# Kernel optimization log

Hardware: AMD Instinct MI355X
Metric: run time of the kernel (lower is better)

The kernel has to match this reference:

```python
import jax, jax.numpy as jnp
import numpy as np

BH, W, C, NHEAD = 512, 256, 128, 4
HEAD_DIM = C // NHEAD
EPS = 1e-5


def _xavier(key, shape):
    fan_out, fan_in = shape
    lim = np.sqrt(6.0 / (fan_in + fan_out)).astype(np.float32)
    return jax.random.uniform(key, shape, jnp.float32, -lim, lim)


def setup_inputs() -> dict:
    key = jax.random.key(0)
    ks = jax.random.split(key, 4)
    return {
        "feat_left": jax.random.normal(ks[0], (BH, W, C), jnp.float32),
        "feat_right": jax.random.normal(ks[1], (BH, W, C), jnp.float32),
        "l_proj_weight": _xavier(ks[2], (2 * C, C)),
        "r_proj_weight": _xavier(ks[3], (2 * C, C)),
        "l_proj_bias": jnp.zeros((2 * C,), jnp.float32),
        "r_proj_bias": jnp.zeros((2 * C,), jnp.float32),
        "l_out_weight": _xavier(jax.random.fold_in(key, 10), (C, C)),
        "l_out_bias": jnp.zeros((C,), jnp.float32),
        "r_out_weight": _xavier(jax.random.fold_in(key, 11), (C, C)),
        "r_out_bias": jnp.zeros((C,), jnp.float32),
        "norm_weight": jnp.ones((C,), jnp.float32),
        "norm_bias": jnp.zeros((C,), jnp.float32),
    }


def _layernorm(x, w, b):
    mu = jnp.mean(x, axis=-1, keepdims=True)
    var = jnp.mean(jnp.square(x - mu), axis=-1, keepdims=True)
    return (x - mu) * jax.lax.rsqrt(var + EPS) * w + b


def reference(feat_left, feat_right, l_proj_weight, r_proj_weight,
              l_proj_bias, r_proj_bias, l_out_weight, l_out_bias,
              r_out_weight, r_out_bias, norm_weight, norm_bias):
    bh, w, c = feat_left.shape
    e, hd = NHEAD, HEAD_DIM

    l_n = _layernorm(feat_left, norm_weight, norm_bias)
    r_n = _layernorm(feat_right, norm_weight, norm_bias)

    l_kv = l_n @ l_proj_weight.T + l_proj_bias
    r_kv = r_n @ r_proj_weight.T + r_proj_bias
    l_k, l_v = jnp.split(l_kv, 2, axis=-1)
    r_k, r_v = jnp.split(r_kv, 2, axis=-1)

    l_k = l_k.reshape(bh, w, e, hd)
    r_k = r_k.reshape(bh, w, e, hd)
    l_v = l_v.reshape(bh, w, e, hd)
    r_v = r_v.reshape(bh, w, e, hd)

    # shared score matrix [bh, heads, w_left, w_right]
    attn = jnp.einsum('nwec,nvec->newv', l_k, r_k) * 0.1

    # left attends over right positions (softmax over last axis)
    sm_l = jax.nn.softmax(attn, axis=-1)
    out_l = jnp.einsum('newv,nvec->nwec', sm_l, r_v).reshape(bh, w, c)

    # right attends over left positions (softmax over w axis of same scores)
    sm_r = jax.nn.softmax(attn, axis=2)
    out_r = jnp.einsum('newv,nwec->nvec', sm_r, l_v).reshape(bh, w, c)

    out_l = out_l @ l_out_weight.T + l_out_bias
    out_r = out_r @ r_out_weight.T + r_out_bias

    return feat_left + out_l, feat_right + out_r
```

## Files before the change

kernel.cpp:

```cpp
#include <hip/hip_runtime.h>
#include <hip/hip_bf16.h>

#define BH   512
#define NW   256
#define CC   128
#define TOK  (BH * NW)

typedef __attribute__((ext_vector_type(8))) short short8;
typedef __attribute__((ext_vector_type(4))) float f32x4;
typedef __attribute__((ext_vector_type(4))) int   i32x4;
typedef __attribute__((ext_vector_type(4))) unsigned short us4;
typedef __attribute__((ext_vector_type(2))) unsigned int u32x2;
typedef unsigned short ushort_t;

static __device__ __forceinline__ f32x4 mfma16(short8 a, short8 b, f32x4 c) {
    return __builtin_amdgcn_mfma_f32_16x16x32_bf16(a, b, c, 0, 0, 0);
}

static __device__ __forceinline__ unsigned int pk2(float a, float b) {
    __hip_bfloat162 h = __float22bfloat162_rn(make_float2(a, b));
    return *reinterpret_cast<unsigned int*>(&h);
}
static __device__ __forceinline__ ushort_t f2bf(float f) {
    unsigned int u = __float_as_uint(f);
    u = (u + 0x7fffu + ((u >> 16) & 1u)) >> 16;
    return (ushort_t)u;
}
#if __has_builtin(__builtin_amdgcn_exp2f)
static __device__ __forceinline__ float exp2_fast(float x) { return __builtin_amdgcn_exp2f(x); }
#else
static __device__ __forceinline__ float exp2_fast(float x) { return exp2f(x); }
#endif

__global__ __launch_bounds__(256)
void k_prep(const float* __restrict__ WpL, const float* __restrict__ WpR,
            const float* __restrict__ bpL, const float* __restrict__ bpR,
            const float* __restrict__ WoL, const float* __restrict__ WoR,
            const float* __restrict__ nw,  const float* __restrict__ nb,
            ushort_t* __restrict__ Wb, float* __restrict__ bias2,
            ushort_t* __restrict__ WoB)
{
    if (blockIdx.x < 8) {
        const int gid = blockIdx.x * 256 + threadIdx.x;
        const int row = gid >> 2;
        const int q   = gid & 3;
        const int side = row >> 8;
        const int o    = row & 255;
        const float* Wp = side ? WpR : WpL;
        const float* bp = side ? bpR : bpL;
        const float* wr = Wp + (size_t)o * 128 + q * 32;

        float acc = 0.f;
#pragma unroll
        for (int g = 0; g < 4; ++g) {
            const int c = q * 32 + g * 8;
            float4 wa = *(const float4*)(wr + g * 8);
            float4 wb = *(const float4*)(wr + g * 8 + 4);
            float4 ga = *(const float4*)(nw + c);
            float4 gb = *(const float4*)(nw + c + 4);
            float4 ba = *(const float4*)(nb + c);
            float4 bb = *(const float4*)(nb + c + 4);
            acc += wa.x*ba.x + wa.y*ba.y + wa.z*ba.z + wa.w*ba.w
                 + wb.x*bb.x + wb.y*bb.y + wb.z*bb.z + wb.w*bb.w;
            u32x2 o0, o1;
            o0[0] = pk2(wa.x*ga.x, wa.y*ga.y);
            o0[1] = pk2(wa.z*ga.z, wa.w*ga.w);
            o1[0] = pk2(wb.x*gb.x, wb.y*gb.y);
            o1[1] = pk2(wb.z*gb.z, wb.w*gb.w);
            *(u32x2*)(Wb + (size_t)row * 128 + c)     = o0;
            *(u32x2*)(Wb + (size_t)row * 128 + c + 4) = o1;
        }
        acc += __shfl_xor(acc, 1);
        acc += __shfl_xor(acc, 2);
        if (q == 0) bias2[row] = bp[o] + acc;
    } else {
        const int idx  = (blockIdx.x - 8) * 256 + threadIdx.x;
        const int row2 = idx >> 2;
        const int q    = idx & 3;
        const int side = row2 >> 7;
        const int o    = row2 & 127;
        const float* Wo = side ? WoR : WoL;
        const float* wr = Wo + (size_t)o * 128 + q * 32;
#pragma unroll
        for (int g = 0; g < 4; ++g) {
            float4 wa = *(const float4*)(wr + g * 8);
            float4 wb = *(const float4*)(wr + g * 8 + 4);
            u32x2 o0, o1;
            o0[0] = pk2(wa.x, wa.y); o0[1] = pk2(wa.z, wa.w);
            o1[0] = pk2(wb.x, wb.y); o1[1] = pk2(wb.z, wb.w);
            *(u32x2*)(WoB + (size_t)row2 * 128 + q * 32 + g * 8)     = o0;
            *(u32x2*)(WoB + (size_t)row2 * 128 + q * 32 + g * 8 + 4) = o1;
        }
    }
}

__global__ __launch_bounds__(512)
void k_ln_proj(const float* __restrict__ featL, const float* __restrict__ featR,
               const ushort_t* __restrict__ Wb, const float* __restrict__ bias2,
               ushort_t* __restrict__ kvL,      ushort_t* __restrict__ kvR)
{
    const int side = blockIdx.y;
    const float* feat = side ? featR : featL;
    const ushort_t* W = Wb + side * 32768;
    const float* b2   = bias2 + side * 256;
    ushort_t*    kv   = side ? kvR : kvL;

    const int m0  = blockIdx.x * 64;
    const int tid = threadIdx.x;
    const int wid = tid >> 6, lane = tid & 63, l16 = lane & 15, lh = lane >> 4;
    const int wn  = wid * 32;

    __shared__ ushort_t Asm[64][136];
    __shared__ ushort_t kvS[64][260];

    const int row = tid >> 3, q = tid & 7;
    const float* fr = feat + (size_t)(m0 + row) * CC + q * 16;
    float x[16];
#pragma unroll
    for (int i = 0; i < 4; ++i) {
        float4 v = *(const float4*)(fr + i * 4);
        x[i*4+0]=v.x; x[i*4+1]=v.y; x[i*4+2]=v.z; x[i*4+3]=v.w;
    }

    short8 Bf[8];
#pragma unroll
    for (int kk = 0; kk < 4; ++kk)
#pragma unroll
        for (int tn = 0; tn < 2; ++tn)
            Bf[kk*2 + tn] = *(const short8*)(W + (size_t)(wn + tn*16 + l16) * CC + kk*32 + lh*8);
    float4 bias[2];
#pragma unroll
    for (int tn = 0; tn < 2; ++tn)
        bias[tn] = *(const float4*)(b2 + wn + tn*16 + lh*4);

    {
        float s = 0.f, s2 = 0.f;
#pragma unroll
        for (int i = 0; i < 16; ++i) { s += x[i]; s2 += x[i]*x[i]; }
#pragma unroll
        for (int m = 1; m < 8; m <<= 1) { s += __shfl_xor(s, m); s2 += __shfl_xor(s2, m); }
        float mu   = s * (1.f / 128.f);
        float var  = s2 * (1.f / 128.f) - mu * mu;
        float rstd = rsqrtf(var + 1e-5f);
        float a = rstd, bsh = -mu * rstd;
#pragma unroll
        for (int g = 0; g < 2; ++g) {
            i32x4 o;
#pragma unroll
            for (int k = 0; k < 4; ++k)
                o[k] = (int)pk2(x[g*8 + 2*k] * a + bsh, x[g*8 + 2*k + 1] * a + bsh);
            *(i32x4*)&Asm[row][q * 16 + g * 8] = o;
        }
    }
    __syncthreads();

    f32x4 acc[4][2];
#pragma unroll
    for (int mt = 0; mt < 4; ++mt)
#pragma unroll
        for (int tn = 0; tn < 2; ++tn)
            acc[mt][tn] = (f32x4){0.f, 0.f, 0.f, 0.f};

#pragma unroll
    for (int kk = 0; kk < 4; ++kk) {
        short8 a[4];
#pragma unroll
        for (int mt = 0; mt < 4; ++mt)
            a[mt] = *(const short8*)&Asm[mt*16 + l16][kk*32 + lh*8];
#pragma unroll
        for (int tn = 0; tn < 2; ++tn)
#pragma unroll
            for (int mt = 0; mt < 4; ++mt)
                acc[mt][tn] = mfma16(Bf[kk*2 + tn], a[mt], acc[mt][tn]);
    }

    const float kscale = (side == 0 && wn < 128) ? 0.14426950408889634f : 1.0f;
#pragma unroll
    for (int mt = 0; mt < 4; ++mt)
#pragma unroll
        for (int tn = 0; tn < 2; ++tn) {
            const int r    = mt*16 + l16;
            const int slot = (wn >> 2) + tn*4 + lh;
            float v0 = (acc[mt][tn][0] + bias[tn].x) * kscale;
            float v1 = (acc[mt][tn][1] + bias[tn].y) * kscale;
            float v2 = (acc[mt][tn][2] + bias[tn].z) * kscale;
            float v3 = (acc[mt][tn][3] + bias[tn].w) * kscale;
            u32x2 wv;
            wv[0] = pk2(v0, v1);
            wv[1] = pk2(v2, v3);
            *(u32x2*)&kvS[r][slot * 4] = wv;
        }
    __syncthreads();

#pragma unroll
    for (int it = 0; it < 8; ++it) {
        int u = it * 512 + tid;
        int r = u >> 6, sl = u & 63;
        u32x2 wv = *(const u32x2*)&kvS[r][sl * 4];
        *(u32x2*)(kv + (size_t)(m0 + r) * 256 + sl * 4) = wv;
    }
}

template<int BF16OUT>
__global__ __launch_bounds__(512, 4)
void k_attn(const ushort_t* __restrict__ kvL, const ushort_t* __restrict__ kvR,
            float* __restrict__ outFBase, ushort_t* __restrict__ outBBase)
{
    const int bx   = blockIdx.x;
    const int work = (bx & 7) * 512 + (bx >> 3);
    const int n    = work >> 3;
    const int e    = (work >> 1) & 3;
    const int dir  = work & 1;
    const ushort_t* kvA = dir ? kvR : kvL;
    const ushort_t* kvB = dir ? kvL : kvR;

    const int tid = threadIdx.x;
    const int wid = tid >> 6, lane = tid & 63, l16 = lane & 15, lh = lane >> 4;
    const int W0 = wid * 32;
    const int kcls = (l16 >> 1) & 3;

    __shared__ ushort_t kB[256][32];
    __shared__ ushort_t vT[32][280];
    __shared__ ushort_t pL[8][32][32];

    {
        const ushort_t* src = kvB + (size_t)n * 256 * 256 + e * 32;
#pragma unroll
        for (int p = 0; p < 2; ++p) {
            int u = tid + p * 512;
            int r = u >> 2, slot = u & 3;
            *(i32x4*)&kB[r][(slot ^ ((r >> 1) & 3)) << 3] =
                *(const i32x4*)(src + (size_t)r * 256 + slot * 8);
        }
    }
    {
        const ushort_t* src = kvB + (size_t)n * 256 * 256 + 128 + e * 32;
#pragma unroll
        for (int u4 = 0; u4 < 4; ++u4) {
            int unit = tid + u4 * 512;
            int cp = unit & 15, vp = unit >> 4;
            unsigned int w0 = *(const unsigned int*)(src + (size_t)(vp*2    ) * 256 + cp*2);
            unsigned int w1 = *(const unsigned int*)(src + (size_t)(vp*2 + 1) * 256 + cp*2);
            *(unsigned int*)&vT[cp*2    ][vp*2] = (w0 & 0xffffu) | (w1 << 16);
            *(unsigned int*)&vT[cp*2 + 1][vp*2] = (w0 >> 16) | (w1 & 0xffff0000u);
        }
    }
    short8 aK[2];
#pragma unroll
    for (int tr = 0; tr < 2; ++tr)
        aK[tr] = *(const short8*)(kvA + (size_t)(n*256 + W0 + tr*16 + l16) * 256 + e*32 + lh*8);

    short8 ones;
#pragma unroll
    for (int i = 0; i < 8; ++i) ones[i] = (short)0x3F80;

    __syncthreads();

    f32x4 oacc[2][2];
#pragma unroll
    for (int tr = 0; tr < 2; ++tr)
#pragma unroll
        for (int ct = 0; ct < 2; ++ct)
            oacc[tr][ct] = (f32x4){0.f, 0.f, 0.f, 0.f};
    f32x4 lacc[2] = {(f32x4){0.f,0.f,0.f,0.f}, (f32x4){0.f,0.f,0.f,0.f}};

#pragma unroll 2
    for (int nc = 0; nc < 8; ++nc) {
        const int vc0 = nc * 32;

        short8 bk0 = *(const short8*)&kB[vc0      + l16][(lh ^ kcls) << 3];
        short8 bk1 = *(const short8*)&kB[vc0 + 16 + l16][(lh ^ kcls) << 3];
        f32x4 s[2][2];
#pragma unroll
        for (int tr = 0; tr < 2; ++tr) {
            s[tr][0] = mfma16(bk0, aK[tr], (f32x4){0.f,0.f,0.f,0.f});
            s[tr][1] = mfma16(bk1, aK[tr], (f32x4){0.f,0.f,0.f,0.f});
        }

#pragma unroll
        for (int tr = 0; tr < 2; ++tr) {
            const int prow = tr*16 + l16;
#pragma unroll
            for (int tc = 0; tc < 2; ++tc) {
                float p0 = exp2_fast(s[tr][tc][0]);
                float p1 = exp2_fast(s[tr][tc][1]);
                float p2 = exp2_fast(s[tr][tc][2]);
                float p3 = exp2_fast(s[tr][tc][3]);
                u32x2 w;
                w[0] = pk2(p0, p1);
                w[1] = pk2(p2, p3);
                const int sL   = 2*tc + (lh >> 1);
                const int pcol = ((sL ^ kcls) << 3) + ((lh & 1) << 2);
                *(u32x2*)&pL[wid][prow][pcol] = w;
            }
        }

        short8 aP[2], bV[2];
#pragma unroll
        for (int tr = 0; tr < 2; ++tr)
            aP[tr] = *(const short8*)&pL[wid][tr*16 + l16][(lh ^ kcls) << 3];
#pragma unroll
        for (int ct = 0; ct < 2; ++ct)
            bV[ct] = *(const short8*)&vT[ct*16 + l16][vc0 + lh*8];
#pragma unroll
        for (int tr = 0; tr < 2; ++tr) {
#pragma unroll
            for (int ct = 0; ct < 2; ++ct)
                oacc[tr][ct] = mfma16(bV[ct], aP[tr], oacc[tr][ct]);
            lacc[tr] = mfma16(ones, aP[tr], lacc[tr]);
        }
    }

#pragma unroll
    for (int tr = 0; tr < 2; ++tr) {
        float rinv = 1.f / lacc[tr][0];
        const int token = n * 256 + W0 + tr*16 + l16;
        if (BF16OUT) {
            ushort_t* outB = outBBase + (size_t)dir * TOK * CC;
#pragma unroll
            for (int ct = 0; ct < 2; ++ct) {
                us4 o;
#pragma unroll
                for (int j = 0; j < 4; ++j)
                    o[j] = f2bf(oacc[tr][ct][j] * rinv);
                *(us4*)(outB + (size_t)token * CC + e*32 + ct*16 + lh*4) = o;
            }
        } else {
            float* outF = outFBase + (size_t)dir * TOK * CC;
#pragma unroll
            for (int ct = 0; ct < 2; ++ct) {
                float4 o;
                o.x = oacc[tr][ct][0] * rinv;
                o.y = oacc[tr][ct][1] * rinv;
                o.z = oacc[tr][ct][2] * rinv;
                o.w = oacc[tr][ct][3] * rinv;
                *(float4*)(outF + (size_t)token * CC + e*32 + ct*16 + lh*4) = o;
            }
        }
    }
}

__global__ __launch_bounds__(512)
void k_outproj_fast(float* __restrict__ outBase, const ushort_t* __restrict__ aoutBase,
                    const float* __restrict__ featL, const float* __restrict__ featR,
                    const ushort_t* __restrict__ WoB,
                    const float* __restrict__ boL, const float* __restrict__ boR)
{
    const int side = blockIdx.y;
    float* io = outBase + (size_t)side * TOK * CC;
    const float* feat = side ? featR : featL;
    const ushort_t* Wo = WoB + side * 16384;
    const float* bo   = side ? boR : boL;

    const int m0 = blockIdx.x * 64;
    const int tid = threadIdx.x;
    const int wid = tid >> 6, lane = tid & 63, l16 = lane & 15, lh = lane >> 4;
    const int wm = (wid >> 2) * 32;
    const int wn = (wid & 3) * 32;

    __shared__ ushort_t Asm[64][136];

    short8 Bf[8];
#pragma unroll
    for (int kk = 0; kk < 4; ++kk)
#pragma unroll
        for (int tn = 0; tn < 2; ++tn)
            Bf[kk*2 + tn] = *(const short8*)(Wo + (size_t)(wn + tn*16 + l16) * CC + kk*32 + lh*8);
    float4 bias4[2];
#pragma unroll
    for (int nt = 0; nt < 2; ++nt)
        bias4[nt] = *(const float4*)(bo + wn + nt*16 + lh*4);

    {
        const ushort_t* src = aoutBase + (size_t)side * TOK * CC;
#pragma unroll
        for (int i = 0; i < 2; ++i) {
            int u = tid + i * 512;
            int r = u >> 4, c0 = (u & 15) * 8;
            *(i32x4*)&Asm[r][c0] = *(const i32x4*)(src + (size_t)(m0 + r) * CC + c0);
        }
    }
    __syncthreads();

    f32x4 acc[2][2];
#pragma unroll
    for (int tr = 0; tr < 2; ++tr)
#pragma unroll
        for (int nt = 0; nt < 2; ++nt)
            acc[tr][nt] = (f32x4){0.f, 0.f, 0.f, 0.f};

#pragma unroll
    for (int kk = 0; kk < 4; ++kk) {
        short8 a[2];
#pragma unroll
        for (int tr = 0; tr < 2; ++tr)
            a[tr] = *(const short8*)&Asm[wm + tr*16 + l16][kk*32 + lh*8];
#pragma unroll
        for (int tr = 0; tr < 2; ++tr)
#pragma unroll
            for (int nt = 0; nt < 2; ++nt)
                acc[tr][nt] = mfma16(Bf[kk*2 + nt], a[tr], acc[tr][nt]);
    }

#pragma unroll
    for (int tr = 0; tr < 2; ++tr) {
        const int token = m0 + wm + tr*16 + l16;
#pragma unroll
        for (int nt = 0; nt < 2; ++nt) {
            const int f0 = wn + nt*16 + lh*4;
            float4 ff = *(const float4*)(feat + (size_t)token * CC + f0);
            float4 o;
            o.x = acc[tr][nt][0] + bias4[nt].x + ff.x;
            o.y = acc[tr][nt][1] + bias4[nt].y + ff.y;
            o.z = acc[tr][nt][2] + bias4[nt].z + ff.z;
            o.w = acc[tr][nt][3] + bias4[nt].w + ff.w;
            *(float4*)(io + (size_t)token * CC + f0) = o;
        }
    }
}

__global__ __launch_bounds__(512, 4)
void k_outproj_slow(float* __restrict__ outBase,
                    const float* __restrict__ featL, const float* __restrict__ featR,
                    const float* __restrict__ WoL,   const float* __restrict__ WoR,
                    const float* __restrict__ boL,   const float* __restrict__ boR)
{
    const int side = blockIdx.y;
    float* io = outBase + (size_t)side * TOK * CC;
    const float* feat = side ? featR : featL;
    const float* Wo   = side ? WoR   : WoL;
    const float* bo   = side ? boR   : boL;

    const int m0 = blockIdx.x * 64;
    const int tid = threadIdx.x;
    const int wid = tid >> 6, lane = tid & 63, l16 = lane & 15, lh = lane >> 4;
    const int wm = (wid >> 2) * 32;
    const int wn = (wid & 3) * 32;

    __shared__ ushort_t Asm[64][136];
    __shared__ ushort_t Wsm[128][136];

    float4 bias4[2];
#pragma unroll
    for (int nt = 0; nt < 2; ++nt)
        bias4[nt] = *(const float4*)(bo + wn + nt*16 + lh*4);

#pragma unroll
    for (int i = 0; i < 8; ++i) {
        int u = tid + i * 512;
        int r = u >> 5, c4 = (u & 31) * 4;
        float4 w4 = *(const float4*)(Wo + (size_t)r * CC + c4);
        u32x2 wv; wv[0] = pk2(w4.x, w4.y); wv[1] = pk2(w4.z, w4.w);
        *(u32x2*)&Wsm[r][c4] = wv;
    }
#pragma unroll
    for (int i = 0; i < 4; ++i) {
        int u = tid + i * 512;
        int r = u >> 5, c4 = (u & 31) * 4;
        float4 a4 = *(const float4*)(io + (size_t)(m0 + r) * CC + c4);
        u32x2 av; av[0] = pk2(a4.x, a4.y); av[1] = pk2(a4.z, a4.w);
        *(u32x2*)&Asm[r][c4] = av;
    }
    __syncthreads();

    f32x4 acc[2][2];
#pragma unroll
    for (int tr = 0; tr < 2; ++tr)
#pragma unroll
        for (int nt = 0; nt < 2; ++nt)
            acc[tr][nt] = (f32x4){0.f, 0.f, 0.f, 0.f};

#pragma unroll
    for (int kk = 0; kk < 4; ++kk) {
        short8 a[2], b[2];
#pragma unroll
        for (int tr = 0; tr < 2; ++tr)
            a[tr] = *(const short8*)&Asm[wm + tr*16 + l16][kk*32 + lh*8];
#pragma unroll
        for (int nt = 0; nt < 2; ++nt)
            b[nt] = *(const short8*)&Wsm[wn + nt*16 + l16][kk*32 + lh*8];
#pragma unroll
        for (int tr = 0; tr < 2; ++tr)
#pragma unroll
            for (int nt = 0; nt < 2; ++nt)
                acc[tr][nt] = mfma16(b[nt], a[tr], acc[tr][nt]);
    }

#pragma unroll
    for (int tr = 0; tr < 2; ++tr) {
        const int token = m0 + wm + tr*16 + l16;
#pragma unroll
        for (int nt = 0; nt < 2; ++nt) {
            const int f0 = wn + nt*16 + lh*4;
            float4 ff = *(const float4*)(feat + (size_t)token * CC + f0);
            float4 o;
            o.x = acc[tr][nt][0] + bias4[nt].x + ff.x;
            o.y = acc[tr][nt][1] + bias4[nt].y + ff.y;
            o.z = acc[tr][nt][2] + bias4[nt].z + ff.z;
            o.w = acc[tr][nt][3] + bias4[nt].w + ff.w;
            *(float4*)(io + (size_t)token * CC + f0) = o;
        }
    }
}

extern "C" void kernel_launch(void* const* d_in, const int* in_sizes, int n_in,
                              void* d_out, int out_size, void* d_ws, size_t ws_size,
                              hipStream_t stream)
{
    const float* featL = (const float*)d_in[0];
    const float* featR = (const float*)d_in[1];
    const float* WpL   = (const float*)d_in[2];
    const float* WpR   = (const float*)d_in[3];
    const float* bpL   = (const float*)d_in[4];
    const float* bpR   = (const float*)d_in[5];
    const float* WoL   = (const float*)d_in[6];
    const float* boL   = (const float*)d_in[7];
    const float* WoR   = (const float*)d_in[8];
    const float* boR   = (const float*)d_in[9];
    const float* nw    = (const float*)d_in[10];
    const float* nb    = (const float*)d_in[11];

    float* out = (float*)d_out;
    ushort_t* kvL = (ushort_t*)d_ws;
    ushort_t* kvR = kvL + (size_t)TOK * 256;
    ushort_t* aout = kvR + (size_t)TOK * 256;

    const size_t kv_us   = (size_t)TOK * 256 * 2;
    const size_t aout_us = (size_t)TOK * CC * 2;
    const size_t wscr_us = 65536 + 1024 + 32768;
    const bool bf16path = ws_size >= (kv_us + aout_us + wscr_us) * 2;

    if (bf16path) {
        ushort_t* Wb  = aout + aout_us;
        float* bias2  = (float*)(Wb + 65536);
        ushort_t* WoB = (ushort_t*)(bias2 + 512);

        k_prep<<<dim3(12), 256, 0, stream>>>(WpL, WpR, bpL, bpR, WoL, WoR,
                                             nw, nb, Wb, bias2, WoB);
        k_ln_proj<<<dim3(2048, 2), 512, 0, stream>>>(featL, featR, Wb, bias2, kvL, kvR);
        k_attn<1><<<dim3(4096), 512, 0, stream>>>(kvL, kvR, out, aout);
        k_outproj_fast<<<dim3(TOK / 64, 2), 512, 0, stream>>>(out, aout, featL, featR,
                                                              WoB, boL, boR);
    } else {
        ushort_t* Wb  = (ushort_t*)d_out;
        float* bias2  = (float*)d_out + 32768;
        ushort_t* WoB = (ushort_t*)d_out + 66560;

        k_prep<<<dim3(12), 256, 0, stream>>>(WpL, WpR, bpL, bpR, WoL, WoR,
                                             nw, nb, Wb, bias2, WoB);
        k_ln_proj<<<dim3(2048, 2), 512, 0, stream>>>(featL, featR, Wb, bias2, kvL, kvR);
        k_attn<0><<<dim3(4096), 512, 0, stream>>>(kvL, kvR, out, aout);
        k_outproj_slow<<<dim3(TOK / 64, 2), 512, 0, stream>>>(out, featL, featR,
                                                              WoL, WoR, boL, boR);
    }
}
```

Baseline: 207.5 us.

## Process four row tiles per block with register prefetch in projection kernels

```diff
diff --git a/kernel.cpp b/kernel.cpp
--- a/kernel.cpp
+++ b/kernel.cpp
@@ -105,7 +105,7 @@
     const float* b2   = bias2 + side * 256;
     ushort_t*    kv   = side ? kvR : kvL;
 
-    const int m0  = blockIdx.x * 64;
+    const int tile0 = blockIdx.x * 4;
     const int tid = threadIdx.x;
     const int wid = tid >> 6, lane = tid & 63, l16 = lane & 15, lh = lane >> 4;
     const int wn  = wid * 32;
@@ -114,12 +114,15 @@
     __shared__ ushort_t kvS[64][260];
 
     const int row = tid >> 3, q = tid & 7;
-    const float* fr = feat + (size_t)(m0 + row) * CC + q * 16;
-    float x[16];
-#pragma unroll
-    for (int i = 0; i < 4; ++i) {
-        float4 v = *(const float4*)(fr + i * 4);
-        x[i*4+0]=v.x; x[i*4+1]=v.y; x[i*4+2]=v.z; x[i*4+3]=v.w;
+
+    float xc[16], xn[16];
+    {
+        const float* fr = feat + (size_t)(tile0 * 64 + row) * CC + q * 16;
+#pragma unroll
+        for (int i = 0; i < 4; ++i) {
+            float4 v = *(const float4*)(fr + i * 4);
+            xc[i*4+0]=v.x; xc[i*4+1]=v.y; xc[i*4+2]=v.z; xc[i*4+3]=v.w;
+        }
     }
 
     short8 Bf[8];
@@ -133,71 +136,91 @@
     for (int tn = 0; tn < 2; ++tn)
         bias[tn] = *(const float4*)(b2 + wn + tn*16 + lh*4);
 
-    {
-        float s = 0.f, s2 = 0.f;
-#pragma unroll
-        for (int i = 0; i < 16; ++i) { s += x[i]; s2 += x[i]*x[i]; }
-#pragma unroll
-        for (int m = 1; m < 8; m <<= 1) { s += __shfl_xor(s, m); s2 += __shfl_xor(s2, m); }
-        float mu   = s * (1.f / 128.f);
-        float var  = s2 * (1.f / 128.f) - mu * mu;
-        float rstd = rsqrtf(var + 1e-5f);
-        float a = rstd, bsh = -mu * rstd;
-#pragma unroll
-        for (int g = 0; g < 2; ++g) {
-            i32x4 o;
-#pragma unroll
-            for (int k = 0; k < 4; ++k)
-                o[k] = (int)pk2(x[g*8 + 2*k] * a + bsh, x[g*8 + 2*k + 1] * a + bsh);
-            *(i32x4*)&Asm[row][q * 16 + g * 8] = o;
-        }
-    }
-    __syncthreads();
-
-    f32x4 acc[4][2];
-#pragma unroll
-    for (int mt = 0; mt < 4; ++mt)
-#pragma unroll
-        for (int tn = 0; tn < 2; ++tn)
-            acc[mt][tn] = (f32x4){0.f, 0.f, 0.f, 0.f};
-
-#pragma unroll
-    for (int kk = 0; kk < 4; ++kk) {
-        short8 a[4];
+    const float kscale = (side == 0 && wn < 128) ? 0.14426950408889634f : 1.0f;
+
+#pragma unroll
+    for (int t = 0; t < 4; ++t) {
+        const int m0 = (tile0 + t) * 64;
+
+        {
+            float s = 0.f, s2 = 0.f;
+#pragma unroll
+            for (int i = 0; i < 16; ++i) { s += xc[i]; s2 += xc[i]*xc[i]; }
+#pragma unroll
+            for (int m = 1; m < 8; m <<= 1) { s += __shfl_xor(s, m); s2 += __shfl_xor(s2, m); }
+            float mu   = s * (1.f / 128.f);
+            float var  = s2 * (1.f / 128.f) - mu * mu;
+            float rstd = rsqrtf(var + 1e-5f);
+            float a = rstd, bsh = -mu * rstd;
+#pragma unroll
+            for (int g = 0; g < 2; ++g) {
+                i32x4 o;
+#pragma unroll
+                for (int k = 0; k < 4; ++k)
+                    o[k] = (int)pk2(xc[g*8 + 2*k] * a + bsh, xc[g*8 + 2*k + 1] * a + bsh);
+                *(i32x4*)&Asm[row][q * 16 + g * 8] = o;
+            }
+        }
+        __syncthreads();
+
+        if (t < 3) {
+            const float* fr = feat + (size_t)(m0 + 64 + row) * CC + q * 16;
+#pragma unroll
+            for (int i = 0; i < 4; ++i) {
+                float4 v = *(const float4*)(fr + i * 4);
+                xn[i*4+0]=v.x; xn[i*4+1]=v.y; xn[i*4+2]=v.z; xn[i*4+3]=v.w;
+            }
+        }
+
+        f32x4 acc[4][2];
 #pragma unroll
         for (int mt = 0; mt < 4; ++mt)
-            a[mt] = *(const short8*)&Asm[mt*16 + l16][kk*32 + lh*8];
-#pragma unroll
-        for (int tn = 0; tn < 2; ++tn)
+#pragma unroll
+            for (int tn = 0; tn < 2; ++tn)
+                acc[mt][tn] = (f32x4){0.f, 0.f, 0.f, 0.f};
+
+#pragma unroll
+        for (int kk = 0; kk < 4; ++kk) {
+            short8 a[4];
 #pragma unroll
             for (int mt = 0; mt < 4; ++mt)
-                acc[mt][tn] = mfma16(Bf[kk*2 + tn], a[mt], acc[mt][tn]);
-    }
-
-    const float kscale = (side == 0 && wn < 128) ? 0.14426950408889634f : 1.0f;
-#pragma unroll
-    for (int mt = 0; mt < 4; ++mt)
-#pragma unroll
-        for (int tn = 0; tn < 2; ++tn) {
-            const int r    = mt*16 + l16;
-            const int slot = (wn >> 2) + tn*4 + lh;
-            float v0 = (acc[mt][tn][0] + bias[tn].x) * kscale;
-            float v1 = (acc[mt][tn][1] + bias[tn].y) * kscale;
-            float v2 = (acc[mt][tn][2] + bias[tn].z) * kscale;
-            float v3 = (acc[mt][tn][3] + bias[tn].w) * kscale;
-            u32x2 wv;
-            wv[0] = pk2(v0, v1);
-            wv[1] = pk2(v2, v3);
-            *(u32x2*)&kvS[r][slot * 4] = wv;
-        }
-    __syncthreads();
-
-#pragma unroll
-    for (int it = 0; it < 8; ++it) {
-        int u = it * 512 + tid;
-        int r = u >> 6, sl = u & 63;
-        u32x2 wv = *(const u32x2*)&kvS[r][sl * 4];
-        *(u32x2*)(kv + (size_t)(m0 + r) * 256 + sl * 4) = wv;
+                a[mt] = *(const short8*)&Asm[mt*16 + l16][kk*32 + lh*8];
+#pragma unroll
+            for (int tn = 0; tn < 2; ++tn)
+#pragma unroll
+                for (int mt = 0; mt < 4; ++mt)
+                    acc[mt][tn] = mfma16(Bf[kk*2 + tn], a[mt], acc[mt][tn]);
+        }
+
+#pragma unroll
+        for (int mt = 0; mt < 4; ++mt)
+#pragma unroll
+            for (int tn = 0; tn < 2; ++tn) {
+                const int r    = mt*16 + l16;
+                const int slot = (wn >> 2) + tn*4 + lh;
+                float v0 = (acc[mt][tn][0] + bias[tn].x) * kscale;
+                float v1 = (acc[mt][tn][1] + bias[tn].y) * kscale;
+                float v2 = (acc[mt][tn][2] + bias[tn].z) * kscale;
+                float v3 = (acc[mt][tn][3] + bias[tn].w) * kscale;
+                u32x2 wv;
+                wv[0] = pk2(v0, v1);
+                wv[1] = pk2(v2, v3);
+                *(u32x2*)&kvS[r][slot * 4] = wv;
+            }
+        __syncthreads();
+
+#pragma unroll
+        for (int it = 0; it < 8; ++it) {
+            int u = it * 512 + tid;
+            int r = u >> 6, sl = u & 63;
+            u32x2 wv = *(const u32x2*)&kvS[r][sl * 4];
+            *(u32x2*)(kv + (size_t)(m0 + r) * 256 + sl * 4) = wv;
+        }
+
+        if (t < 3) {
+#pragma unroll
+            for (int i = 0; i < 16; ++i) xc[i] = xn[i];
+        }
     }
 }
 
@@ -351,14 +374,15 @@
     const float* feat = side ? featR : featL;
     const ushort_t* Wo = WoB + side * 16384;
     const float* bo   = side ? boR : boL;
-
-    const int m0 = blockIdx.x * 64;
+    const ushort_t* src = aoutBase + (size_t)side * TOK * CC;
+
+    const int tile0 = blockIdx.x * 4;
     const int tid = threadIdx.x;
     const int wid = tid >> 6, lane = tid & 63, l16 = lane & 15, lh = lane >> 4;
     const int wm = (wid >> 2) * 32;
     const int wn = (wid & 3) * 32;
 
-    __shared__ ushort_t Asm[64][136];
+    __shared__ ushort_t Asm[2][64][136];
 
     short8 Bf[8];
 #pragma unroll
@@ -371,50 +395,76 @@
     for (int nt = 0; nt < 2; ++nt)
         bias4[nt] = *(const float4*)(bo + wn + nt*16 + lh*4);
 
-    {
-        const ushort_t* src = aoutBase + (size_t)side * TOK * CC;
+    i32x4 aReg[2];
+#pragma unroll
+    for (int i = 0; i < 2; ++i) {
+        int u = tid + i * 512;
+        int r = u >> 4, c0 = (u & 15) * 8;
+        aReg[i] = *(const i32x4*)(src + (size_t)(tile0 * 64 + r) * CC + c0);
+    }
+
+#pragma unroll
+    for (int t = 0; t < 4; ++t) {
+        const int m0 = (tile0 + t) * 64;
+        const int p  = t & 1;
+
 #pragma unroll
         for (int i = 0; i < 2; ++i) {
             int u = tid + i * 512;
             int r = u >> 4, c0 = (u & 15) * 8;
-            *(i32x4*)&Asm[r][c0] = *(const i32x4*)(src + (size_t)(m0 + r) * CC + c0);
-        }
-    }
-    __syncthreads();
-
-    f32x4 acc[2][2];
-#pragma unroll
-    for (int tr = 0; tr < 2; ++tr)
-#pragma unroll
-        for (int nt = 0; nt < 2; ++nt)
-            acc[tr][nt] = (f32x4){0.f, 0.f, 0.f, 0.f};
-
-#pragma unroll
-    for (int kk = 0; kk < 4; ++kk) {
-        short8 a[2];
+            *(i32x4*)&Asm[p][r][c0] = aReg[i];
+        }
+        __syncthreads();
+
+        if (t < 3) {
+#pragma unroll
+            for (int i = 0; i < 2; ++i) {
+                int u = tid + i * 512;
+                int r = u >> 4, c0 = (u & 15) * 8;
+                aReg[i] = *(const i32x4*)(src + (size_t)(m0 + 64 + r) * CC + c0);
+            }
+        }
+        float4 ff[2][2];
 #pragma unroll
         for (int tr = 0; tr < 2; ++tr)
-            a[tr] = *(const short8*)&Asm[wm + tr*16 + l16][kk*32 + lh*8];
+#pragma unroll
+            for (int nt = 0; nt < 2; ++nt)
+                ff[tr][nt] = *(const float4*)(feat + (size_t)(m0 + wm + tr*16 + l16) * CC
+                                              + wn + nt*16 + lh*4);
+
+        f32x4 acc[2][2];
 #pragma unroll
         for (int tr = 0; tr < 2; ++tr)
 #pragma unroll
             for (int nt = 0; nt < 2; ++nt)
-                acc[tr][nt] = mfma16(Bf[kk*2 + nt], a[tr], acc[tr][nt]);
-    }
-
-#pragma unroll
-    for (int tr = 0; tr < 2; ++tr) {
-        const int token = m0 + wm + tr*16 + l16;
-#pragma unroll
-        for (int nt = 0; nt < 2; ++nt) {
-            const int f0 = wn + nt*16 + lh*4;
-            float4 ff = *(const float4*)(feat + (size_t)token * CC + f0);
-            float4 o;
-            o.x = acc[tr][nt][0] + bias4[nt].x + ff.x;
-            o.y = acc[tr][nt][1] + bias4[nt].y + ff.y;
-            o.z = acc[tr][nt][2] + bias4[nt].z + ff.z;
-            o.w = acc[tr][nt][3] + bias4[nt].w + ff.w;
-            *(float4*)(io + (size_t)token * CC + f0) = o;
+                acc[tr][nt] = (f32x4){0.f, 0.f, 0.f, 0.f};
+
+#pragma unroll
+        for (int kk = 0; kk < 4; ++kk) {
+            short8 a[2];
+#pragma unroll
+            for (int tr = 0; tr < 2; ++tr)
+                a[tr] = *(const short8*)&Asm[p][wm + tr*16 + l16][kk*32 + lh*8];
+#pragma unroll
+            for (int tr = 0; tr < 2; ++tr)
+#pragma unroll
+                for (int nt = 0; nt < 2; ++nt)
+                    acc[tr][nt] = mfma16(Bf[kk*2 + nt], a[tr], acc[tr][nt]);
+        }
+
+#pragma unroll
+        for (int tr = 0; tr < 2; ++tr) {
+            const int token = m0 + wm + tr*16 + l16;
+#pragma unroll
+            for (int nt = 0; nt < 2; ++nt) {
+                const int f0 = wn + nt*16 + lh*4;
+                float4 o;
+                o.x = acc[tr][nt][0] + bias4[nt].x + ff[tr][nt].x;
+                o.y = acc[tr][nt][1] + bias4[nt].y + ff[tr][nt].y;
+                o.z = acc[tr][nt][2] + bias4[nt].z + ff[tr][nt].z;
+                o.w = acc[tr][nt][3] + bias4[nt].w + ff[tr][nt].w;
+                *(float4*)(io + (size_t)token * CC + f0) = o;
+            }
         }
     }
 }
@@ -537,10 +587,10 @@
 
         k_prep<<<dim3(12), 256, 0, stream>>>(WpL, WpR, bpL, bpR, WoL, WoR,
                                              nw, nb, Wb, bias2, WoB);
-        k_ln_proj<<<dim3(2048, 2), 512, 0, stream>>>(featL, featR, Wb, bias2, kvL, kvR);
+        k_ln_proj<<<dim3(512, 2), 512, 0, stream>>>(featL, featR, Wb, bias2, kvL, kvR);
         k_attn<1><<<dim3(4096), 512, 0, stream>>>(kvL, kvR, out, aout);
-        k_outproj_fast<<<dim3(TOK / 64, 2), 512, 0, stream>>>(out, aout, featL, featR,
-                                                              WoB, boL, boR);
+        k_outproj_fast<<<dim3(512, 2), 512, 0, stream>>>(out, aout, featL, featR,
+                                                         WoB, boL, boR);
     } else {
         ushort_t* Wb  = (ushort_t*)d_out;
         float* bias2  = (float*)d_out + 32768;
@@ -548,7 +598,7 @@
 
         k_prep<<<dim3(12), 256, 0, stream>>>(WpL, WpR, bpL, bpR, WoL, WoR,
                                              nw, nb, Wb, bias2, WoB);
-        k_ln_proj<<<dim3(2048, 2), 512, 0, stream>>>(featL, featR, Wb, bias2, kvL, kvR);
+        k_ln_proj<<<dim3(512, 2), 512, 0, stream>>>(featL, featR, Wb, bias2, kvL, kvR);
         k_attn<0><<<dim3(4096), 512, 0, stream>>>(kvL, kvR, out, aout);
         k_outproj_slow<<<dim3(TOK / 64, 2), 512, 0, stream>>>(out, featL, featR,
                                                               WoL, WoR, boL, boR);
```

Result: faster. 196.7 us (-5.2%).

## Fuse output projection into attention kernel, looping heads per block

Applied to the files above, without the earlier changes.

```diff
diff --git a/kernel.cpp b/kernel.cpp
--- a/kernel.cpp
+++ b/kernel.cpp
@@ -110,8 +110,9 @@
     const int wid = tid >> 6, lane = tid & 63, l16 = lane & 15, lh = lane >> 4;
     const int wn  = wid * 32;
 
-    __shared__ ushort_t Asm[64][136];
-    __shared__ ushort_t kvS[64][260];
+    __shared__ ushort_t smem[64 * 260];
+    ushort_t (*Asm)[136] = (ushort_t (*)[136])smem;
+    ushort_t (*kvS)[260] = (ushort_t (*)[260])smem;
 
     const int row = tid >> 3, q = tid & 7;
     const float* fr = feat + (size_t)(m0 + row) * CC + q * 16;
@@ -173,6 +174,7 @@
             for (int mt = 0; mt < 4; ++mt)
                 acc[mt][tn] = mfma16(Bf[kk*2 + tn], a[mt], acc[mt][tn]);
     }
+    __syncthreads();
 
     const float kscale = (side == 0 && wn < 128) ? 0.14426950408889634f : 1.0f;
 #pragma unroll
@@ -201,10 +203,179 @@
     }
 }
 
-template<int BF16OUT>
+__global__ __launch_bounds__(256)
+void k_attn_fused(const ushort_t* __restrict__ kvL, const ushort_t* __restrict__ kvR,
+                  const float* __restrict__ featL, const float* __restrict__ featR,
+                  const ushort_t* __restrict__ WoB,
+                  const float* __restrict__ boL, const float* __restrict__ boR,
+                  float* __restrict__ outBase)
+{
+    const int bx   = blockIdx.x;
+    const int work = (bx & 7) * 256 + (bx >> 3);
+    const int n    = work >> 2;
+    const int h    = (work >> 1) & 1;
+    const int dir  = work & 1;
+    const ushort_t* kvA = dir ? kvR : kvL;
+    const ushort_t* kvB = dir ? kvL : kvR;
+    const float* feat = dir ? featR : featL;
+    const ushort_t* Wo = WoB + dir * 16384;
+    const float* bo   = dir ? boR : boL;
+    float* io = outBase + (size_t)dir * TOK * CC;
+
+    const int tid = threadIdx.x;
+    const int wid = tid >> 6, lane = tid & 63, l16 = lane & 15, lh = lane >> 4;
+    const int W0 = h * 128 + wid * 32;
+    const int kcls = (l16 >> 1) & 3;
+
+    __shared__ ushort_t kB[256][32];
+    __shared__ ushort_t vT[32][280];
+    __shared__ ushort_t pL[4][32][32];
+
+    short8 ones;
+#pragma unroll
+    for (int i = 0; i < 8; ++i) ones[i] = (short)0x3F80;
+
+    f32x4 acc2[2][8];
+#pragma unroll
+    for (int tr = 0; tr < 2; ++tr)
+#pragma unroll
+        for (int ft = 0; ft < 8; ++ft)
+            acc2[tr][ft] = (f32x4){0.f, 0.f, 0.f, 0.f};
+
+    for (int e = 0; e < 4; ++e) {
+        if (e) __syncthreads();
+
+        {
+            const ushort_t* src = kvB + (size_t)n * 65536 + e * 32;
+#pragma unroll
+            for (int p = 0; p < 4; ++p) {
+                int u = tid + p * 256;
+                int r = u >> 2, slot = u & 3;
+                *(i32x4*)&kB[r][(slot ^ ((r >> 1) & 3)) << 3] =
+                    *(const i32x4*)(src + (size_t)r * 256 + slot * 8);
+            }
+        }
+        {
+            const ushort_t* src = kvB + (size_t)n * 65536 + 128 + e * 32;
+#pragma unroll
+            for (int u4 = 0; u4 < 8; ++u4) {
+                int unit = tid + u4 * 256;
+                int cp = unit & 15, vp = unit >> 4;
+                unsigned int w0 = *(const unsigned int*)(src + (size_t)(vp*2    ) * 256 + cp*2);
+                unsigned int w1 = *(const unsigned int*)(src + (size_t)(vp*2 + 1) * 256 + cp*2);
+                *(unsigned int*)&vT[cp*2    ][vp*2] = (w0 & 0xffffu) | (w1 << 16);
+                *(unsigned int*)&vT[cp*2 + 1][vp*2] = (w0 >> 16) | (w1 & 0xffff0000u);
+            }
+        }
+        short8 aK[2];
+#pragma unroll
+        for (int tr = 0; tr < 2; ++tr)
+            aK[tr] = *(const short8*)(kvA + (size_t)(n*256 + W0 + tr*16 + l16) * 256 + e*32 + lh*8);
+
+        __syncthreads();
+
+        f32x4 oacc[2][2];
+#pragma unroll
+        for (int tr = 0; tr < 2; ++tr)
+#pragma unroll
+            for (int ct = 0; ct < 2; ++ct)
+                oacc[tr][ct] = (f32x4){0.f, 0.f, 0.f, 0.f};
+        f32x4 lacc[2] = {(f32x4){0.f,0.f,0.f,0.f}, (f32x4){0.f,0.f,0.f,0.f}};
+
+#pragma unroll 2
+        for (int nc = 0; nc < 8; ++nc) {
+            const int vc0 = nc * 32;
+
+            short8 bk0 = *(const short8*)&kB[vc0      + l16][(lh ^ kcls) << 3];
+            short8 bk1 = *(const short8*)&kB[vc0 + 16 + l16][(lh ^ kcls) << 3];
+            f32x4 s[2][2];
+#pragma unroll
+            for (int tr = 0; tr < 2; ++tr) {
+                s[tr][0] = mfma16(bk0, aK[tr], (f32x4){0.f,0.f,0.f,0.f});
+                s[tr][1] = mfma16(bk1, aK[tr], (f32x4){0.f,0.f,0.f,0.f});
+            }
+
+#pragma unroll
+            for (int tr = 0; tr < 2; ++tr) {
+                const int prow = tr*16 + l16;
+#pragma unroll
+                for (int tc = 0; tc < 2; ++tc) {
+                    float p0 = exp2_fast(s[tr][tc][0]);
+                    float p1 = exp2_fast(s[tr][tc][1]);
+                    float p2 = exp2_fast(s[tr][tc][2]);
+                    float p3 = exp2_fast(s[tr][tc][3]);
+                    u32x2 w;
+                    w[0] = pk2(p0, p1);
+                    w[1] = pk2(p2, p3);
+                    const int sL   = 2*tc + (lh >> 1);
+                    const int pcol = ((sL ^ kcls) << 3) + ((lh & 1) << 2);
+                    *(u32x2*)&pL[wid][prow][pcol] = w;
+                }
+            }
+
+            short8 aP[2], bV[2];
+#pragma unroll
+            for (int tr = 0; tr < 2; ++tr)
+                aP[tr] = *(const short8*)&pL[wid][tr*16 + l16][(lh ^ kcls) << 3];
+#pragma unroll
+            for (int ct = 0; ct < 2; ++ct)
+                bV[ct] = *(const short8*)&vT[ct*16 + l16][vc0 + lh*8];
+#pragma unroll
+            for (int tr = 0; tr < 2; ++tr) {
+#pragma unroll
+                for (int ct = 0; ct < 2; ++ct)
+                    oacc[tr][ct] = mfma16(bV[ct], aP[tr], oacc[tr][ct]);
+                lacc[tr] = mfma16(ones, aP[tr], lacc[tr]);
+            }
+        }
+
+#pragma unroll
+        for (int tr = 0; tr < 2; ++tr) {
+            float rinv = 1.f / lacc[tr][0];
+            const int prow = tr*16 + l16;
+#pragma unroll
+            for (int tc = 0; tc < 2; ++tc) {
+                u32x2 w;
+                w[0] = pk2(oacc[tr][tc][0] * rinv, oacc[tr][tc][1] * rinv);
+                w[1] = pk2(oacc[tr][tc][2] * rinv, oacc[tr][tc][3] * rinv);
+                const int sL   = 2*tc + (lh >> 1);
+                const int pcol = ((sL ^ kcls) << 3) + ((lh & 1) << 2);
+                *(u32x2*)&pL[wid][prow][pcol] = w;
+            }
+        }
+
+#pragma unroll
+        for (int tr = 0; tr < 2; ++tr) {
+            short8 aP2 = *(const short8*)&pL[wid][tr*16 + l16][(lh ^ kcls) << 3];
+#pragma unroll
+            for (int ft = 0; ft < 8; ++ft) {
+                short8 wf = *(const short8*)(Wo + (size_t)(ft*16 + l16) * CC + e*32 + lh*8);
+                acc2[tr][ft] = mfma16(wf, aP2, acc2[tr][ft]);
+            }
+        }
+    }
+
+#pragma unroll
+    for (int tr = 0; tr < 2; ++tr) {
+        const int token = n * 256 + W0 + tr*16 + l16;
+#pragma unroll
+        for (int ft = 0; ft < 8; ++ft) {
+            const int f0 = ft*16 + lh*4;
+            float4 bo4 = *(const float4*)(bo + f0);
+            float4 ff  = *(const float4*)(feat + (size_t)token * CC + f0);
+            float4 o;
+            o.x = acc2[tr][ft][0] + bo4.x + ff.x;
+            o.y = acc2[tr][ft][1] + bo4.y + ff.y;
+            o.z = acc2[tr][ft][2] + bo4.z + ff.z;
+            o.w = acc2[tr][ft][3] + bo4.w + ff.w;
+            *(float4*)(io + (size_t)token * CC + f0) = o;
+        }
+    }
+}
+
 __global__ __launch_bounds__(512, 4)
-void k_attn(const ushort_t* __restrict__ kvL, const ushort_t* __restrict__ kvR,
-            float* __restrict__ outFBase, ushort_t* __restrict__ outBBase)
+void k_attn_f32(const ushort_t* __restrict__ kvL, const ushort_t* __restrict__ kvR,
+                float* __restrict__ outFBase)
 {
     const int bx   = blockIdx.x;
     const int work = (bx & 7) * 512 + (bx >> 3);
@@ -224,7 +395,7 @@
     __shared__ ushort_t pL[8][32][32];
 
     {
-        const ushort_t* src = kvB + (size_t)n * 256 * 256 + e * 32;
+        const ushort_t* src = kvB + (size_t)n * 65536 + e * 32;
 #pragma unroll
         for (int p = 0; p < 2; ++p) {
             int u = tid + p * 512;
@@ -234,7 +405,7 @@
         }
     }
     {
-        const ushort_t* src = kvB + (size_t)n * 256 * 256 + 128 + e * 32;
+        const ushort_t* src = kvB + (size_t)n * 65536 + 128 + e * 32;
 #pragma unroll
         for (int u4 = 0; u4 < 4; ++u4) {
             int unit = tid + u4 * 512;
@@ -267,7 +438,6 @@
 #pragma unroll 2
     for (int nc = 0; nc < 8; ++nc) {
         const int vc0 = nc * 32;
-
         short8 bk0 = *(const short8*)&kB[vc0      + l16][(lh ^ kcls) << 3];
         short8 bk1 = *(const short8*)&kB[vc0 + 16 + l16][(lh ^ kcls) << 3];
         f32x4 s[2][2];
@@ -276,7 +446,6 @@
             s[tr][0] = mfma16(bk0, aK[tr], (f32x4){0.f,0.f,0.f,0.f});
             s[tr][1] = mfma16(bk1, aK[tr], (f32x4){0.f,0.f,0.f,0.f});
         }
-
 #pragma unroll
         for (int tr = 0; tr < 2; ++tr) {
             const int prow = tr*16 + l16;
@@ -294,7 +463,6 @@
                 *(u32x2*)&pL[wid][prow][pcol] = w;
             }
         }
-
         short8 aP[2], bV[2];
 #pragma unroll
         for (int tr = 0; tr < 2; ++tr)
@@ -315,106 +483,15 @@
     for (int tr = 0; tr < 2; ++tr) {
         float rinv = 1.f / lacc[tr][0];
         const int token = n * 256 + W0 + tr*16 + l16;
-        if (BF16OUT) {
-            ushort_t* outB = outBBase + (size_t)dir * TOK * CC;
-#pragma unroll
-            for (int ct = 0; ct < 2; ++ct) {
-                us4 o;
-#pragma unroll
-                for (int j = 0; j < 4; ++j)
-                    o[j] = f2bf(oacc[tr][ct][j] * rinv);
-                *(us4*)(outB + (size_t)token * CC + e*32 + ct*16 + lh*4) = o;
-            }
-        } else {
-            float* outF = outFBase + (size_t)dir * TOK * CC;
-#pragma unroll
-            for (int ct = 0; ct < 2; ++ct) {
-                float4 o;
-                o.x = oacc[tr][ct][0] * rinv;
-                o.y = oacc[tr][ct][1] * rinv;
-                o.z = oacc[tr][ct][2] * rinv;
-                o.w = oacc[tr][ct][3] * rinv;
-                *(float4*)(outF + (size_t)token * CC + e*32 + ct*16 + lh*4) = o;
-            }
-        }
-    }
-}
-
-__global__ __launch_bounds__(512)
-void k_outproj_fast(float* __restrict__ outBase, const ushort_t* __restrict__ aoutBase,
-                    const float* __restrict__ featL, const float* __restrict__ featR,
-                    const ushort_t* __restrict__ WoB,
-                    const float* __restrict__ boL, const float* __restrict__ boR)
-{
-    const int side = blockIdx.y;
-    float* io = outBase + (size_t)side * TOK * CC;
-    const float* feat = side ? featR : featL;
-    const ushort_t* Wo = WoB + side * 16384;
-    const float* bo   = side ? boR : boL;
-
-    const int m0 = blockIdx.x * 64;
-    const int tid = threadIdx.x;
-    const int wid = tid >> 6, lane = tid & 63, l16 = lane & 15, lh = lane >> 4;
-    const int wm = (wid >> 2) * 32;
-    const int wn = (wid & 3) * 32;
-
-    __shared__ ushort_t Asm[64][136];
-
-    short8 Bf[8];
-#pragma unroll
-    for (int kk = 0; kk < 4; ++kk)
-#pragma unroll
-        for (int tn = 0; tn < 2; ++tn)
-            Bf[kk*2 + tn] = *(const short8*)(Wo + (size_t)(wn + tn*16 + l16) * CC + kk*32 + lh*8);
-    float4 bias4[2];
-#pragma unroll
-    for (int nt = 0; nt < 2; ++nt)
-        bias4[nt] = *(const float4*)(bo + wn + nt*16 + lh*4);
-
-    {
-        const ushort_t* src = aoutBase + (size_t)side * TOK * CC;
-#pragma unroll
-        for (int i = 0; i < 2; ++i) {
-            int u = tid + i * 512;
-            int r = u >> 4, c0 = (u & 15) * 8;
-            *(i32x4*)&Asm[r][c0] = *(const i32x4*)(src + (size_t)(m0 + r) * CC + c0);
-        }
-    }
-    __syncthreads();
-
-    f32x4 acc[2][2];
-#pragma unroll
-    for (int tr = 0; tr < 2; ++tr)
-#pragma unroll
-        for (int nt = 0; nt < 2; ++nt)
-            acc[tr][nt] = (f32x4){0.f, 0.f, 0.f, 0.f};
-
-#pragma unroll
-    for (int kk = 0; kk < 4; ++kk) {
-        short8 a[2];
-#pragma unroll
-        for (int tr = 0; tr < 2; ++tr)
-            a[tr] = *(const short8*)&Asm[wm + tr*16 + l16][kk*32 + lh*8];
-#pragma unroll
-        for (int tr = 0; tr < 2; ++tr)
-#pragma unroll
-            for (int nt = 0; nt < 2; ++nt)
-                acc[tr][nt] = mfma16(Bf[kk*2 + nt], a[tr], acc[tr][nt]);
-    }
-
-#pragma unroll
-    for (int tr = 0; tr < 2; ++tr) {
-        const int token = m0 + wm + tr*16 + l16;
-#pragma unroll
-        for (int nt = 0; nt < 2; ++nt) {
-            const int f0 = wn + nt*16 + lh*4;
-            float4 ff = *(const float4*)(feat + (size_t)token * CC + f0);
+        float* outF = outFBase + (size_t)dir * TOK * CC;
+#pragma unroll
+        for (int ct = 0; ct < 2; ++ct) {
             float4 o;
-            o.x = acc[tr][nt][0] + bias4[nt].x + ff.x;
-            o.y = acc[tr][nt][1] + bias4[nt].y + ff.y;
-            o.z = acc[tr][nt][2] + bias4[nt].z + ff.z;
-            o.w = acc[tr][nt][3] + bias4[nt].w + ff.w;
-            *(float4*)(io + (size_t)token * CC + f0) = o;
+            o.x = oacc[tr][ct][0] * rinv;
+            o.y = oacc[tr][ct][1] * rinv;
+            o.z = oacc[tr][ct][2] * rinv;
+            o.w = oacc[tr][ct][3] * rinv;
+            *(float4*)(outF + (size_t)token * CC + e*32 + ct*16 + lh*4) = o;
         }
     }
 }
@@ -523,24 +600,21 @@
     float* out = (float*)d_out;
     ushort_t* kvL = (ushort_t*)d_ws;
     ushort_t* kvR = kvL + (size_t)TOK * 256;
-    ushort_t* aout = kvR + (size_t)TOK * 256;
 
     const size_t kv_us   = (size_t)TOK * 256 * 2;
-    const size_t aout_us = (size_t)TOK * CC * 2;
     const size_t wscr_us = 65536 + 1024 + 32768;
-    const bool bf16path = ws_size >= (kv_us + aout_us + wscr_us) * 2;
-
-    if (bf16path) {
-        ushort_t* Wb  = aout + aout_us;
+    const bool fusedpath = ws_size >= (kv_us * 2 + wscr_us) * 2;
+
+    if (fusedpath) {
+        ushort_t* Wb  = kvR + (size_t)TOK * 256;
         float* bias2  = (float*)(Wb + 65536);
         ushort_t* WoB = (ushort_t*)(bias2 + 512);
 
         k_prep<<<dim3(12), 256, 0, stream>>>(WpL, WpR, bpL, bpR, WoL, WoR,
                                              nw, nb, Wb, bias2, WoB);
         k_ln_proj<<<dim3(2048, 2), 512, 0, stream>>>(featL, featR, Wb, bias2, kvL, kvR);
-        k_attn<1><<<dim3(4096), 512, 0, stream>>>(kvL, kvR, out, aout);
-        k_outproj_fast<<<dim3(TOK / 64, 2), 512, 0, stream>>>(out, aout, featL, featR,
-                                                              WoB, boL, boR);
+        k_attn_fused<<<dim3(2048), 256, 0, stream>>>(kvL, kvR, featL, featR,
+                                                     WoB, boL, boR, out);
     } else {
         ushort_t* Wb  = (ushort_t*)d_out;
         float* bias2  = (float*)d_out + 32768;
@@ -549,7 +623,7 @@
         k_prep<<<dim3(12), 256, 0, stream>>>(WpL, WpR, bpL, bpR, WoL, WoR,
                                              nw, nb, Wb, bias2, WoB);
         k_ln_proj<<<dim3(2048, 2), 512, 0, stream>>>(featL, featR, Wb, bias2, kvL, kvR);
-        k_attn<0><<<dim3(4096), 512, 0, stream>>>(kvL, kvR, out, aout);
+        k_attn_f32<<<dim3(4096), 512, 0, stream>>>(kvL, kvR, out);
         k_outproj_slow<<<dim3(TOK / 64, 2), 512, 0, stream>>>(out, featL, featR,
                                                               WoL, WoR, boL, boR);
     }
```

New measurement: 231.0 us. 11.4% more time.
